# Optimization experiments

Hardware: AMD Instinct MI355X
Metric: run time of the kernel (lower is better)

## Reference

```python
import jax, jax.numpy as jnp
import numpy as np

B, S, I, H = 32, 512, 256, 512  # batch, seq, input, lstm hidden
E = 2 * H                       # embed = hidden*2
NH = 16                         # num heads
HD = E // NH                    # head dim = 64


def setup_inputs() -> dict:
    key = jax.random.key(0)
    ks = jax.random.split(key, 20)
    sI = 1.0 / np.sqrt(I)
    sH = 1.0 / np.sqrt(H)
    sE = 1.0 / np.sqrt(E)
    return {
        "x": jax.random.normal(ks[0], (B, S, I), jnp.float32),
        # LSTM params (PyTorch gate order i,f,g,o); b = b_ih + b_hh folded
        "W_ih_f": jax.random.uniform(ks[1], (4 * H, I), jnp.float32, -sH, sH),
        "W_hh_f": jax.random.uniform(ks[2], (4 * H, H), jnp.float32, -sH, sH),
        "b_f": jax.random.uniform(ks[3], (4 * H,), jnp.float32, -sH, sH),
        "W_ih_b": jax.random.uniform(ks[4], (4 * H, I), jnp.float32, -sH, sH),
        "W_hh_b": jax.random.uniform(ks[5], (4 * H, H), jnp.float32, -sH, sH),
        "b_b": jax.random.uniform(ks[6], (4 * H,), jnp.float32, -sH, sH),
        # attention projections
        "Wq": jax.random.uniform(ks[7], (E, E), jnp.float32, -sE, sE),
        "bq": jax.random.uniform(ks[8], (E,), jnp.float32, -sE, sE),
        "Wk": jax.random.uniform(ks[9], (E, E), jnp.float32, -sE, sE),
        "bk": jax.random.uniform(ks[10], (E,), jnp.float32, -sE, sE),
        "Wv": jax.random.uniform(ks[11], (E, E), jnp.float32, -sE, sE),
        "bv": jax.random.uniform(ks[12], (E,), jnp.float32, -sE, sE),
        "Wo": jax.random.uniform(ks[13], (E, E), jnp.float32, -sE, sE),
        "bo": jax.random.uniform(ks[14], (E,), jnp.float32, -sE, sE),
        # final classifier
        "Wfc": jax.random.uniform(ks[15], (1, E), jnp.float32, -sE, sE),
        "bfc": jax.random.uniform(ks[16], (1,), jnp.float32, -sE, sE),
    }


def _lstm_dir(x, W_ih, W_hh, b, reverse):
    # x: (B,S,I) -> hidden sequence (B,S,H), PyTorch gate order i,f,g,o
    xg = jnp.einsum('bsi,gi->sbg', x, W_ih) + b  # time-major (S,B,4H)
    h0 = jnp.zeros((x.shape[0], W_hh.shape[1]), x.dtype)

    def step(carry, xt):
        h, c = carry
        gates = xt + h @ W_hh.T
        i, f, g, o = jnp.split(gates, 4, axis=-1)
        c = jax.nn.sigmoid(f) * c + jax.nn.sigmoid(i) * jnp.tanh(g)
        h = jax.nn.sigmoid(o) * jnp.tanh(c)
        return (h, c), h

    _, hs = jax.lax.scan(step, (h0, h0), xg, reverse=reverse)
    return jnp.swapaxes(hs, 0, 1)  # (B,S,H)


def reference(x, W_ih_f, W_hh_f, b_f, W_ih_b, W_hh_b, b_b,
              Wq, bq, Wk, bk, Wv, bv, Wo, bo, Wfc, bfc):
    # Bidirectional LSTM
    h_fwd = _lstm_dir(x, W_ih_f, W_hh_f, b_f, reverse=False)
    h_bwd = _lstm_dir(x, W_ih_b, W_hh_b, b_b, reverse=True)
    h = jnp.concatenate([h_fwd, h_bwd], axis=-1)  # (B,S,E)

    # Multi-head attention, replicating the original (label-scrambled) einsums.
    # Q/K/V are reshaped to (N, NH, S, HD) via transpose(1,2) as in torch.
    def proj(W, bias):
        p = h @ W.T + bias                      # (B,S,E)
        return p.reshape(B, S, NH, HD).transpose(0, 2, 1, 3)  # (B,NH,S,HD)

    Q, K, V = proj(Wq, bq), proj(Wk, bk), proj(Wv, bv)
    # torch: einsum('nqhd,nkhd->nhqk', Q, K) with Q,K actually (N,NH,S,HD)
    # => scores shape (B, S, NH, NH), softmax over last (heads) axis
    scores = jnp.einsum('nqhd,nkhd->nhqk', Q, K) / jnp.sqrt(jnp.float32(HD))
    attn = jax.nn.softmax(scores, axis=-1)
    # torch: einsum('nhqk,nkhd->nqhd', attn, V) -> (B, NH, S, HD)
    out = jnp.einsum('nhqk,nkhd->nqhd', attn, V).reshape(B, S, E)
    out = out @ Wo.T + bo                       # (B,S,E)

    # dropout is identity at inference; take last timestep, fc, sigmoid
    last = out[:, -1, :]                        # (B,E)
    return jax.nn.sigmoid(last @ Wfc.T + bfc)   # (B,1)
```

## Files before the change

kernel.cpp:

```cpp
#include <hip/hip_runtime.h>
#include <cstdint>
#include <cstddef>


typedef _Float16 v8h __attribute__((ext_vector_type(8)));
typedef _Float16 v4h __attribute__((ext_vector_type(4)));
typedef float    v4f __attribute__((ext_vector_type(4)));

#define AT_LD(p)     __hip_atomic_load((p), __ATOMIC_RELAXED, __HIP_MEMORY_SCOPE_AGENT)
#define AT_ST(p, v)  __hip_atomic_store((p), (v), __ATOMIC_RELAXED, __HIP_MEMORY_SCOPE_AGENT)

static constexpr size_t OFF_CNT   = 0;
static constexpr size_t OFF_LOGIT = 256;
static constexpr size_t OFF_BEFF  = 512;
static constexpr size_t OFF_WEFF  = 1024;
static constexpr size_t OFF_HF    = 8192;
static constexpr size_t HF_BYTES  = 513ull*32768;
static constexpr size_t OFF_HB    = OFF_HF + HF_BYTES;
static constexpr size_t HB_BYTES  = 17ull*32768;
static constexpr size_t OFF_WHHF  = OFF_HB + HB_BYTES;
static constexpr size_t OFF_WIHF  = OFF_WHHF + 2048ull*512*2;
static constexpr size_t OFF_WHHB  = OFF_WIHF + 2048ull*256*2;
static constexpr size_t OFF_WIHB  = OFF_WHHB + 2048ull*512*2;
static constexpr size_t OFF_WKT   = OFF_WIHB + 2048ull*256*2;
static constexpr size_t OFF_WQT   = OFF_WKT + 1024ull*1024*2;
static constexpr size_t OFF_WV2   = OFF_WQT + 1024ull*64*2;
static constexpr size_t OFF_CV    = OFF_WV2 + 16ull*1024*16*4;

static constexpr int PSTR    = 776;
static constexpr int GSTR    = 68;
static constexpr int LDS_PANEL_B = 16*PSTR*2;
static constexpr int DYN_LDS = LDS_PANEL_B + 64*GSTR*4;

__device__ __forceinline__ bool has_ffff(unsigned long long w) {
    return ((w & 0xFFFFull) == 0xFFFFull) ||
           (((w >> 16) & 0xFFFFull) == 0xFFFFull) ||
           (((w >> 32) & 0xFFFFull) == 0xFFFFull) ||
           ((w >> 48) == 0xFFFFull);
}


__global__ void k_convert(const float* __restrict__ whhf, const float* __restrict__ wihf,
                          const float* __restrict__ whhb, const float* __restrict__ wihb,
                          char* __restrict__ ws)
{
    _Float16* o1 = (_Float16*)(ws + OFF_WHHF);
    _Float16* o2 = (_Float16*)(ws + OFF_WIHF);
    _Float16* o3 = (_Float16*)(ws + OFF_WHHB);
    _Float16* o4 = (_Float16*)(ws + OFF_WIHB);
    const int stride = gridDim.x * blockDim.x;
    for (int i = blockIdx.x*blockDim.x + threadIdx.x; i < 2048*512; i += stride) {
        o1[i] = (_Float16)whhf[i];
        o3[i] = (_Float16)whhb[i];
    }
    for (int i = blockIdx.x*blockDim.x + threadIdx.x; i < 2048*256; i += stride) {
        o2[i] = (_Float16)wihf[i];
        o4[i] = (_Float16)wihb[i];
    }
}

__global__ void k_weff(const float* __restrict__ Wfc, const float* __restrict__ Wo,
                       const float* __restrict__ bo, const float* __restrict__ bfc,
                       char* __restrict__ ws)
{
    float* weff = (float*)(ws + OFF_WEFF);
    float* beff = (float*)(ws + OFF_BEFF);
    const int bid = blockIdx.x;
    const int e2 = (bid & 3)*256 + threadIdx.x;
    const int slab = bid >> 2;
    float a = 0.f;
    for (int e = slab*64; e < slab*64 + 64; ++e)
        a += Wfc[e] * Wo[(size_t)e*1024 + e2];
    atomicAdd(weff + e2, a);
    if ((bid & 3) == 0 && threadIdx.x < 64) {
        const int e = slab*64 + threadIdx.x;
        float b = Wfc[e]*bo[e];
        if (bid == 0 && threadIdx.x == 0) b += bfc[0];
        atomicAdd(beff, b);
    }
}

__global__ void k_wv2(const float* __restrict__ Wv, const float* __restrict__ bv,
                      char* __restrict__ ws)
{
    const float* weff = (const float*)(ws + OFF_WEFF);
    float* wv2 = (float*)(ws + OFF_WV2);
    float* cv  = (float*)(ws + OFF_CV);
    const int bid = blockIdx.x;
    if (bid < 64) {
        const int r = bid >> 2;
        const int e = (bid & 3)*256 + threadIdx.x;
        for (int kh = 0; kh < 16; ++kh) {
            float a = 0.f;
            for (int hd = 0; hd < 64; ++hd)
                a += weff[r*64 + hd] * Wv[((size_t)(kh*64 + hd))*1024 + e];
            wv2[((size_t)r*1024 + e)*16 + kh] = a;
        }
    } else {
        const int r2 = threadIdx.x >> 4, k2 = threadIdx.x & 15;
        float a = 0.f;
        for (int hd = 0; hd < 64; ++hd)
            a += weff[r2*64 + hd] * bv[k2*64 + hd];
        cv[threadIdx.x] = a;
    }
}

__global__ void k_tk(const float* __restrict__ Wk, char* __restrict__ ws)
{
    _Float16* WkT = (_Float16*)(ws + OFF_WKT);
    __shared__ float tile[32][33];
    const int jt = blockIdx.x & 31, et = blockIdx.x >> 5;
    const int tx = threadIdx.x & 31, ty = threadIdx.x >> 5;
    for (int i = 0; i < 4; ++i)
        tile[ty + 8*i][tx] = Wk[((size_t)(jt*32 + ty + 8*i))*1024 + et*32 + tx];
    __syncthreads();
    for (int i = 0; i < 4; ++i)
        WkT[((size_t)(et*32 + ty + 8*i))*1024 + jt*32 + tx] = (_Float16)tile[tx][ty + 8*i];
}

__global__ void k_tq(const float* __restrict__ Wq, char* __restrict__ ws)
{
    _Float16* WqT = (_Float16*)(ws + OFF_WQT);
    const int gid = blockIdx.x*256 + threadIdx.x;
    const int d = gid & 63, e = gid >> 6;
    WqT[e*64 + d] = (_Float16)Wq[((size_t)(960 + d))*1024 + e];
}


__global__ __launch_bounds__(256, 1)
void bilstm_main(const float* __restrict__ xg,
                 const float* __restrict__ b_f, const float* __restrict__ b_b,
                 const float* __restrict__ bq,  const float* __restrict__ bk,
                 char* __restrict__ ws, float* __restrict__ out)
{
    extern __shared__ char smem[];
    _Float16* panel = (_Float16*)smem;
    float* gates = (float*)(smem + LDS_PANEL_B);

    const int tid  = threadIdx.x;
    const int wgid = blockIdx.x;
    const int wave = tid >> 6;
    const int lane = tid & 63;
    const int quad = lane >> 4;
    const int l16  = lane & 15;
    const int grp  = wgid >> 5;
    const int col0 = (wgid & 31) * 16;

    unsigned* cnts  = (unsigned*)(ws + OFF_CNT);
    float*   logits = (float*)(ws + OFF_LOGIT);

    const int ac = tid & 15;
    const int ab = tid >> 4;

    for (int phase = 0; phase < 2; ++phase) {
        const int dir     = phase == 0 ? 1 : 0;
        const int nsteps  = dir ? 16 : 512;
        char* hslab = ws + (dir ? OFF_HB : OFF_HF);
        const _Float16* whh = (const _Float16*)(ws + (dir ? OFF_WHHB : OFF_WHHF));
        const _Float16* wih = (const _Float16*)(ws + (dir ? OFF_WIHB : OFF_WIHF));
        const float* bias = dir ? b_b : b_f;

        v8h bfrag[4][6];
#pragma unroll
        for (int nt = 0; nt < 4; ++nt)
#pragma unroll
            for (int kk = 0; kk < 6; ++kk) {
                const int kb = (wave*6 + kk)*32 + quad*8;
                const int r  = nt*512 + col0 + l16;
                const _Float16* src = (kb < 512) ? (whh + (size_t)r*512 + kb)
                                                 : (wih + (size_t)r*256 + (kb - 512));
                bfrag[nt][kk] = *(const v8h*)src;
            }
        float bia[4];
#pragma unroll
        for (int g = 0; g < 4; ++g) bia[g] = bias[g*512 + col0 + ac];

        float cst = 0.f;

        for (int t = 0; t < nsteps; ++t) {
            const int s = dir ? (511 - t) : t;

            float4 xv[2];
#pragma unroll
            for (int i = 0; i < 2; ++i) {
                const int ch = tid + 256*i;
                const int b = ch >> 6, ic = ch & 63;
                xv[i] = *(const float4*)(xg + ((size_t)(grp*8 + b)*512 + s)*256 + ic*4);
            }

            {
                const int b = tid >> 5, seg = tid & 31;
                const unsigned long long* src = (const unsigned long long*)hslab
                    + (size_t)t*4096 + (size_t)(grp*8 + b)*128 + seg*4;
                unsigned long long w0, w1, w2, w3;
                for (;;) {
                    w0 = AT_LD(src + 0); w1 = AT_LD(src + 1);
                    w2 = AT_LD(src + 2); w3 = AT_LD(src + 3);
                    if (!(has_ffff(w0) || has_ffff(w1) || has_ffff(w2) || has_ffff(w3)))
                        break;
                    __builtin_amdgcn_s_sleep(1);
                }
                unsigned long long* dst = (unsigned long long*)(panel + b*PSTR + seg*16);
                dst[0] = w0; dst[1] = w1; dst[2] = w2; dst[3] = w3;
            }
#pragma unroll
            for (int i = 0; i < 2; ++i) {
                const int ch = tid + 256*i;
                const int b = ch >> 6, ic = ch & 63;
                v4h hx = { (_Float16)xv[i].x, (_Float16)xv[i].y,
                           (_Float16)xv[i].z, (_Float16)xv[i].w };
                *(v4h*)(panel + b*PSTR + 512 + ic*4) = hx;
            }
            __syncthreads();

            v4f acc[4];
#pragma unroll
            for (int nt = 0; nt < 4; ++nt) { v4f z = {0.f,0.f,0.f,0.f}; acc[nt] = z; }
#pragma unroll
            for (int kk = 0; kk < 6; ++kk) {
                const int kb = (wave*6 + kk)*32 + quad*8;
                const v8h a0 = *(const v8h*)(panel + l16*PSTR + kb);
#pragma unroll
                for (int nt = 0; nt < 4; ++nt)
                    acc[nt] = __builtin_amdgcn_mfma_f32_16x16x32_f16(a0, bfrag[nt][kk], acc[nt], 0, 0, 0);
            }
#pragma unroll
            for (int nt = 0; nt < 4; ++nt)
#pragma unroll
                for (int r = 0; r < 4; ++r)
                    gates[(nt*16 + l16)*GSTR + (quad*4 + r)*4 + wave] = acc[nt][r];
            __syncthreads();

            if (tid < 128) {
                float g[4];
#pragma unroll
                for (int gi = 0; gi < 4; ++gi) {
                    const v4f v = *(const v4f*)(gates + (gi*16 + ac)*GSTR + ab*4);
                    g[gi] = v.x + v.y + v.z + v.w + bia[gi];
                }
                const float ig = 1.f/(1.f + __expf(-g[0]));
                const float fg = 1.f/(1.f + __expf(-g[1]));
                const float gg = 1.f - 2.f/(__expf(2.f*g[2]) + 1.f);
                const float og = 1.f/(1.f + __expf(-g[3]));
                cst = fg*cst + ig*gg;
                const float hn = og * (1.f - 2.f/(__expf(2.f*cst) + 1.f));
                const unsigned hb = (unsigned)__builtin_bit_cast(unsigned short, (_Float16)hn);
                const unsigned ot = (unsigned)__shfl_xor((int)hb, 1);
                if ((ac & 1) == 0) {
                    _Float16* hrow = (_Float16*)hslab
                        + ((size_t)(t+1)*32 + (grp*8 + ab))*512 + col0 + ac;
                    AT_ST((unsigned*)hrow, hb | (ot << 16));
                }
            }
        }
    }

    __syncthreads();
    if (tid == 0) {
        __hip_atomic_fetch_add(cnts + 0, 1u, __ATOMIC_RELAXED, __HIP_MEMORY_SCOPE_AGENT);
        while (AT_LD(cnts + 0) < 128u) __builtin_amdgcn_s_sleep(8);
    }
    __syncthreads();

    float*    hv  = (float*)smem;
    _Float16* k16 = (_Float16*)(smem + 16384);
    float*    qb  = (float*)(smem + 24576);
    float*    vzb = (float*)(smem + 25600);
    float*    scb = (float*)(smem + 25856);
    int*      lastf = (int*)(smem + 26112);

    const _Float16* WkT = (const _Float16*)(ws + OFF_WKT);
    const _Float16* WqT = (const _Float16*)(ws + OFF_WQT);
    const float* wv2 = (const float*)(ws + OFF_WV2);
    const float* cv  = (const float*)(ws + OFF_CV);
    const float* beff= (const float*)(ws + OFF_BEFF);

    const int p0 = wgid * 4;
#pragma unroll
    for (int i = 0; i < 4; ++i) {
        const int ch = tid + 256*i;
        const int pp = ch >> 8, q = ch & 255;
        const int p = p0 + pp; const int b = p >> 4; const int r = p & 15;
        unsigned long long w;
        if (q < 128)
            w = AT_LD((const unsigned long long*)(ws + OFF_HF)
                      + ((size_t)(497 + r)*32 + b)*128 + q);
        else
            w = AT_LD((const unsigned long long*)(ws + OFF_HB)
                      + ((size_t)(16 - r)*32 + b)*128 + (q - 128));
        float* dst = hv + pp*1024 + q*4;
#pragma unroll
        for (int j = 0; j < 4; ++j)
            dst[j] = (float)__builtin_bit_cast(_Float16, (unsigned short)((w >> (16*j)) & 0xFFFF));
    }
    __syncthreads();

    float kacc[4][4];
#pragma unroll
    for (int jj = 0; jj < 4; ++jj) {
        const float bkv = bk[jj*256 + tid];
#pragma unroll
        for (int pp = 0; pp < 4; ++pp) kacc[jj][pp] = bkv;
    }
    for (int e = 0; e < 1024; ++e) {
        float hvv[4];
#pragma unroll
        for (int pp = 0; pp < 4; ++pp) hvv[pp] = hv[pp*1024 + e];
#pragma unroll
        for (int jj = 0; jj < 4; ++jj) {
            const float w = (float)WkT[(size_t)e*1024 + jj*256 + tid];
#pragma unroll
            for (int pp = 0; pp < 4; ++pp) kacc[jj][pp] += w * hvv[pp];
        }
    }
#pragma unroll
    for (int jj = 0; jj < 4; ++jj)
#pragma unroll
        for (int pp = 0; pp < 4; ++pp)
            k16[pp*1024 + jj*256 + tid] = (_Float16)kacc[jj][pp];

    {
        const int d = tid & 63, ph = tid >> 6;
        float a0 = bq[960 + d];
        for (int e = 0; e < 1024; ++e)
            a0 += (float)WqT[e*64 + d] * hv[ph*1024 + e];
        qb[ph*64 + d] = a0;
    }
    if (tid < 64) {
        const int pp = tid >> 4, kh = tid & 15;
        const int r = (p0 + pp) & 15;
        float a = cv[r*16 + kh];
        for (int e = 0; e < 1024; ++e)
            a += wv2[((size_t)r*1024 + e)*16 + kh] * hv[pp*1024 + e];
        vzb[pp*16 + kh] = a;
    }
    __syncthreads();
    if (tid < 64) {
        const int pp = tid >> 4, kh = tid & 15;
        float a = 0.f;
#pragma unroll
        for (int d = 0; d < 64; ++d)
            a += qb[pp*64 + d] * (float)k16[pp*1024 + kh*64 + d];
        scb[pp*16 + kh] = a * 0.125f;
    }
    __syncthreads();
    if (tid < 4) {
        const int base = tid*16;
        float m = scb[base];
        for (int kh = 1; kh < 16; ++kh) m = fmaxf(m, scb[base+kh]);
        float sum = 0.f, wz = 0.f;
        for (int kh = 0; kh < 16; ++kh) {
            const float pe = __expf(scb[base+kh] - m);
            sum += pe; wz += pe * vzb[base+kh];
        }
        atomicAdd(&logits[(p0 + tid) >> 4], wz / sum);
    }
    __syncthreads();
    if (tid == 0) {
        const unsigned old = __hip_atomic_fetch_add(cnts + 2, 1u, __ATOMIC_RELAXED, __HIP_MEMORY_SCOPE_AGENT);
        *lastf = (old == 127u) ? 1 : 0;
    }
    __syncthreads();
    if (*lastf) {
        if (tid < 32) {
            const float lg = AT_LD(logits + tid) + beff[0];
            out[tid] = 1.f/(1.f + __expf(-lg));
        }
    }
}


extern "C" void kernel_launch(void* const* d_in, const int* in_sizes, int n_in,
                              void* d_out, int out_size, void* d_ws, size_t ws_size,
                              hipStream_t stream)
{
    (void)in_sizes; (void)n_in; (void)out_size; (void)ws_size;
    const float* x    = (const float*)d_in[0];
    const float* Wihf = (const float*)d_in[1];
    const float* Whhf = (const float*)d_in[2];
    const float* b_f  = (const float*)d_in[3];
    const float* Wihb = (const float*)d_in[4];
    const float* Whhb = (const float*)d_in[5];
    const float* b_b  = (const float*)d_in[6];
    const float* Wq   = (const float*)d_in[7];
    const float* bq   = (const float*)d_in[8];
    const float* Wk   = (const float*)d_in[9];
    const float* bk   = (const float*)d_in[10];
    const float* Wv   = (const float*)d_in[11];
    const float* bv   = (const float*)d_in[12];
    const float* Wo   = (const float*)d_in[13];
    const float* bo   = (const float*)d_in[14];
    const float* Wfc  = (const float*)d_in[15];
    const float* bfc  = (const float*)d_in[16];
    char* ws = (char*)d_ws;
    float* out = (float*)d_out;

    hipMemsetAsync(ws, 0, OFF_HF + 32768, stream);
    hipMemsetAsync(ws + OFF_HF + 32768, 0xFF, 512ull*32768, stream);
    hipMemsetAsync(ws + OFF_HB, 0, 32768, stream);
    hipMemsetAsync(ws + OFF_HB + 32768, 0xFF, 16ull*32768, stream);

    hipLaunchKernelGGL(k_convert, dim3(512), dim3(256), 0, stream, Whhf, Wihf, Whhb, Wihb, ws);
    hipLaunchKernelGGL(k_weff,    dim3(64),  dim3(256), 0, stream, Wfc, Wo, bo, bfc, ws);
    hipLaunchKernelGGL(k_wv2,     dim3(65),  dim3(256), 0, stream, Wv, bv, ws);
    hipLaunchKernelGGL(k_tk,      dim3(1024),dim3(256), 0, stream, Wk, ws);
    hipLaunchKernelGGL(k_tq,      dim3(256), dim3(256), 0, stream, Wq, ws);
    hipLaunchKernelGGL(bilstm_main, dim3(128), dim3(256), DYN_LDS, stream,
                       x, b_f, b_b, bq, bk, ws, out);
}
```

Baseline: 1.853 ms.

## Replace sentinel-polled h slabs with flagged ring buffer and halve workgroups

The recurrent hidden-state exchange no longer uses a full per-timestep slab pre-filled with 0xFFFF sentinels. It now uses a 4-deep ring buffer plus per-step flag words, and each consumer spins on a 64-bit flag pair before reading. The grid drops from 128 to 64 workgroups, each handling 16 batch rows with all 256 threads doing cell updates. The last 16 timesteps are written to a compact history buffer for the attention tail, which removes the large 0xFF memsets. The risks are tighter sync ordering (relying on s_waitcnt plus relaxed atomics), busy-wait loops without sleep, and double the per-workgroup work on the serial critical path.

```diff
diff --git a/kernel.cpp b/kernel.cpp
--- a/kernel.cpp
+++ b/kernel.cpp
@@ -6,6 +6,7 @@
 typedef _Float16 v8h __attribute__((ext_vector_type(8)));
 typedef _Float16 v4h __attribute__((ext_vector_type(4)));
 typedef float    v4f __attribute__((ext_vector_type(4)));
+typedef unsigned long long u64;
 
 #define AT_LD(p)     __hip_atomic_load((p), __ATOMIC_RELAXED, __HIP_MEMORY_SCOPE_AGENT)
 #define AT_ST(p, v)  __hip_atomic_store((p), (v), __ATOMIC_RELAXED, __HIP_MEMORY_SCOPE_AGENT)
@@ -14,11 +15,13 @@
 static constexpr size_t OFF_LOGIT = 256;
 static constexpr size_t OFF_BEFF  = 512;
 static constexpr size_t OFF_WEFF  = 1024;
-static constexpr size_t OFF_HF    = 8192;
-static constexpr size_t HF_BYTES  = 513ull*32768;
-static constexpr size_t OFF_HB    = OFF_HF + HF_BYTES;
-static constexpr size_t HB_BYTES  = 17ull*32768;
-static constexpr size_t OFF_WHHF  = OFF_HB + HB_BYTES;
+static constexpr size_t OFF_FLAGF = 8192;
+static constexpr size_t OFF_FLAGB = OFF_FLAGF + 512ull*64*4;
+static constexpr size_t ZERO_BYTES= OFF_FLAGB + 16ull*64*4;
+static constexpr size_t OFF_RINGF = ZERO_BYTES;
+static constexpr size_t OFF_RINGB = OFF_RINGF + 4ull*2*16*512*2;
+static constexpr size_t OFF_HIST  = OFF_RINGB + 4ull*2*16*512*2;
+static constexpr size_t OFF_WHHF  = OFF_HIST + 32ull*16*1024*4;
 static constexpr size_t OFF_WIHF  = OFF_WHHF + 2048ull*512*2;
 static constexpr size_t OFF_WHHB  = OFF_WIHF + 2048ull*256*2;
 static constexpr size_t OFF_WIHB  = OFF_WHHB + 2048ull*512*2;
@@ -27,17 +30,12 @@
 static constexpr size_t OFF_WV2   = OFF_WQT + 1024ull*64*2;
 static constexpr size_t OFF_CV    = OFF_WV2 + 16ull*1024*16*4;
 
-static constexpr int PSTR    = 776;
-static constexpr int GSTR    = 68;
+static constexpr int PSTR = 776;
+static constexpr int GSTR = 68;
 static constexpr int LDS_PANEL_B = 16*PSTR*2;
-static constexpr int DYN_LDS = LDS_PANEL_B + 64*GSTR*4;
-
-__device__ __forceinline__ bool has_ffff(unsigned long long w) {
-    return ((w & 0xFFFFull) == 0xFFFFull) ||
-           (((w >> 16) & 0xFFFFull) == 0xFFFFull) ||
-           (((w >> 32) & 0xFFFFull) == 0xFFFFull) ||
-           ((w >> 48) == 0xFFFFull);
-}
+static constexpr int LDS_GATES_B = 64*GSTR*4;
+static constexpr int DYN_LDS = 53504;
+static constexpr u64 FLAG_PAIR = 0x0000000100000001ull;
 
 
 __global__ void k_convert(const float* __restrict__ whhf, const float* __restrict__ wihf,
@@ -136,6 +134,7 @@
     extern __shared__ char smem[];
     _Float16* panel = (_Float16*)smem;
     float* gates = (float*)(smem + LDS_PANEL_B);
+    _Float16* hout = (_Float16*)(smem + LDS_PANEL_B + LDS_GATES_B);
 
     const int tid  = threadIdx.x;
     const int wgid = blockIdx.x;
@@ -144,21 +143,25 @@
     const int quad = lane >> 4;
     const int l16  = lane & 15;
     const int grp  = wgid >> 5;
-    const int col0 = (wgid & 31) * 16;
+    const int cg   = wgid & 31;
+    const int col0 = cg * 16;
 
     unsigned* cnts  = (unsigned*)(ws + OFF_CNT);
     float*   logits = (float*)(ws + OFF_LOGIT);
+    float*   hist   = (float*)(ws + OFF_HIST);
 
     const int ac = tid & 15;
     const int ab = tid >> 4;
 
     for (int phase = 0; phase < 2; ++phase) {
-        const int dir     = phase == 0 ? 1 : 0;
-        const int nsteps  = dir ? 16 : 512;
-        char* hslab = ws + (dir ? OFF_HB : OFF_HF);
+        const int dir    = (phase == 0) ? 1 : 0;
+        const int nsteps = dir ? 16 : 512;
+        _Float16* ring = (_Float16*)(ws + (dir ? OFF_RINGB : OFF_RINGF));
+        unsigned* flg  = (unsigned*)(ws + (dir ? OFF_FLAGB : OFF_FLAGF));
         const _Float16* whh = (const _Float16*)(ws + (dir ? OFF_WHHB : OFF_WHHF));
         const _Float16* wih = (const _Float16*)(ws + (dir ? OFF_WIHB : OFF_WIHF));
         const float* bias = dir ? b_b : b_f;
+        const int histoff = dir ? 512 : 0;
 
         v8h bfrag[4][6];
 #pragma unroll
@@ -180,31 +183,32 @@
         for (int t = 0; t < nsteps; ++t) {
             const int s = dir ? (511 - t) : t;
 
-            float4 xv[2];
-#pragma unroll
-            for (int i = 0; i < 2; ++i) {
+            float4 xv[4];
+#pragma unroll
+            for (int i = 0; i < 4; ++i) {
                 const int ch = tid + 256*i;
                 const int b = ch >> 6, ic = ch & 63;
-                xv[i] = *(const float4*)(xg + ((size_t)(grp*8 + b)*512 + s)*256 + ic*4);
-            }
-
-            {
-                const int b = tid >> 5, seg = tid & 31;
-                const unsigned long long* src = (const unsigned long long*)hslab
-                    + (size_t)t*4096 + (size_t)(grp*8 + b)*128 + seg*4;
-                unsigned long long w0, w1, w2, w3;
-                for (;;) {
-                    w0 = AT_LD(src + 0); w1 = AT_LD(src + 1);
-                    w2 = AT_LD(src + 2); w3 = AT_LD(src + 3);
-                    if (!(has_ffff(w0) || has_ffff(w1) || has_ffff(w2) || has_ffff(w3)))
-                        break;
-                    __builtin_amdgcn_s_sleep(1);
-                }
-                unsigned long long* dst = (unsigned long long*)(panel + b*PSTR + seg*16);
-                dst[0] = w0; dst[1] = w1; dst[2] = w2; dst[3] = w3;
-            }
-#pragma unroll
-            for (int i = 0; i < 2; ++i) {
+                xv[i] = *(const float4*)(xg + ((size_t)(grp*16 + b)*512 + s)*256 + ic*4);
+            }
+
+            if (t == 0) {
+                u64* dst = (u64*)(panel + ab*PSTR + ac*32);
+#pragma unroll
+                for (int j = 0; j < 8; ++j) dst[j] = 0ull;
+            } else {
+                const u64* f64 = (const u64*)flg + ((size_t)(t-1)*2 + grp)*16 + ac;
+                while (AT_LD(f64) != FLAG_PAIR) {}
+                const u64* src = (const u64*)ring
+                    + ((((size_t)((t-1) & 3))*2 + grp)*16 + ab)*128 + ac*8;
+                u64 w[8];
+#pragma unroll
+                for (int j = 0; j < 8; ++j) w[j] = AT_LD(src + j);
+                u64* dst = (u64*)(panel + ab*PSTR + ac*32);
+#pragma unroll
+                for (int j = 0; j < 8; ++j) dst[j] = w[j];
+            }
+#pragma unroll
+            for (int i = 0; i < 4; ++i) {
                 const int ch = tid + 256*i;
                 const int b = ch >> 6, ic = ch & 63;
                 v4h hx = { (_Float16)xv[i].x, (_Float16)xv[i].y,
@@ -231,7 +235,7 @@
                     gates[(nt*16 + l16)*GSTR + (quad*4 + r)*4 + wave] = acc[nt][r];
             __syncthreads();
 
-            if (tid < 128) {
+            {
                 float g[4];
 #pragma unroll
                 for (int gi = 0; gi < 4; ++gi) {
@@ -244,13 +248,21 @@
                 const float og = 1.f/(1.f + __expf(-g[3]));
                 cst = fg*cst + ig*gg;
                 const float hn = og * (1.f - 2.f/(__expf(2.f*cst) + 1.f));
-                const unsigned hb = (unsigned)__builtin_bit_cast(unsigned short, (_Float16)hn);
-                const unsigned ot = (unsigned)__shfl_xor((int)hb, 1);
-                if ((ac & 1) == 0) {
-                    _Float16* hrow = (_Float16*)hslab
-                        + ((size_t)(t+1)*32 + (grp*8 + ab))*512 + col0 + ac;
-                    AT_ST((unsigned*)hrow, hb | (ot << 16));
-                }
+                hout[ab*16 + ac] = (_Float16)hn;
+                if (s >= 496)
+                    AT_ST(hist + ((size_t)(grp*16 + ab)*16 + (s - 496))*1024
+                               + histoff + col0 + ac, hn);
+            }
+            __syncthreads();
+
+            if (wave == 0) {
+                const int b = lane >> 2, seg = lane & 3;
+                const u64 v = *(const u64*)(hout + b*16 + seg*4);
+                AT_ST((u64*)(ring + ((((size_t)(t & 3))*2 + grp)*16 + b)*512
+                             + col0 + seg*4), v);
+                asm volatile("s_waitcnt vmcnt(0)" ::: "memory");
+                if (lane == 0)
+                    AT_ST(flg + ((size_t)t*2 + grp)*32 + cg, 1u);
             }
         }
     }
@@ -258,16 +270,16 @@
     __syncthreads();
     if (tid == 0) {
         __hip_atomic_fetch_add(cnts + 0, 1u, __ATOMIC_RELAXED, __HIP_MEMORY_SCOPE_AGENT);
-        while (AT_LD(cnts + 0) < 128u) __builtin_amdgcn_s_sleep(8);
+        while (AT_LD(cnts + 0) < 64u) {}
     }
     __syncthreads();
 
     float*    hv  = (float*)smem;
-    _Float16* k16 = (_Float16*)(smem + 16384);
-    float*    qb  = (float*)(smem + 24576);
-    float*    vzb = (float*)(smem + 25600);
-    float*    scb = (float*)(smem + 25856);
-    int*      lastf = (int*)(smem + 26112);
+    _Float16* k16 = (_Float16*)(smem + 32768);
+    float*    qb  = (float*)(smem + 49152);
+    float*    vzb = (float*)(smem + 51200);
+    float*    scb = (float*)(smem + 51712);
+    int*      lastf = (int*)(smem + 53248);
 
     const _Float16* WkT = (const _Float16*)(ws + OFF_WKT);
     const _Float16* WqT = (const _Float16*)(ws + OFF_WQT);
@@ -275,58 +287,56 @@
     const float* cv  = (const float*)(ws + OFF_CV);
     const float* beff= (const float*)(ws + OFF_BEFF);
 
-    const int p0 = wgid * 4;
-#pragma unroll
-    for (int i = 0; i < 4; ++i) {
-        const int ch = tid + 256*i;
-        const int pp = ch >> 8, q = ch & 255;
-        const int p = p0 + pp; const int b = p >> 4; const int r = p & 15;
-        unsigned long long w;
-        if (q < 128)
-            w = AT_LD((const unsigned long long*)(ws + OFF_HF)
-                      + ((size_t)(497 + r)*32 + b)*128 + q);
-        else
-            w = AT_LD((const unsigned long long*)(ws + OFF_HB)
-                      + ((size_t)(16 - r)*32 + b)*128 + (q - 128));
-        float* dst = hv + pp*1024 + q*4;
-#pragma unroll
-        for (int j = 0; j < 4; ++j)
-            dst[j] = (float)__builtin_bit_cast(_Float16, (unsigned short)((w >> (16*j)) & 0xFFFF));
-    }
-    __syncthreads();
-
-    float kacc[4][4];
+    const int p0 = wgid * 8;
+    {
+        const u64* hist64 = (const u64*)hist;
+#pragma unroll
+        for (int i = 0; i < 16; ++i) {
+            const int ch = tid + 256*i;
+            const int pp = ch >> 9, e2 = ch & 511;
+            const int p = p0 + pp; const int b = p >> 4, r = p & 15;
+            const u64 w = AT_LD(hist64 + ((size_t)b*16 + r)*512 + e2);
+            *(u64*)(hv + pp*1024 + e2*2) = w;
+        }
+    }
+    __syncthreads();
+
+    float kacc[4][8];
 #pragma unroll
     for (int jj = 0; jj < 4; ++jj) {
         const float bkv = bk[jj*256 + tid];
 #pragma unroll
-        for (int pp = 0; pp < 4; ++pp) kacc[jj][pp] = bkv;
+        for (int pp = 0; pp < 8; ++pp) kacc[jj][pp] = bkv;
     }
     for (int e = 0; e < 1024; ++e) {
-        float hvv[4];
-#pragma unroll
-        for (int pp = 0; pp < 4; ++pp) hvv[pp] = hv[pp*1024 + e];
+        float hvv[8];
+#pragma unroll
+        for (int pp = 0; pp < 8; ++pp) hvv[pp] = hv[pp*1024 + e];
 #pragma unroll
         for (int jj = 0; jj < 4; ++jj) {
             const float w = (float)WkT[(size_t)e*1024 + jj*256 + tid];
 #pragma unroll
-            for (int pp = 0; pp < 4; ++pp) kacc[jj][pp] += w * hvv[pp];
+            for (int pp = 0; pp < 8; ++pp) kacc[jj][pp] += w * hvv[pp];
         }
     }
 #pragma unroll
     for (int jj = 0; jj < 4; ++jj)
 #pragma unroll
-        for (int pp = 0; pp < 4; ++pp)
+        for (int pp = 0; pp < 8; ++pp)
             k16[pp*1024 + jj*256 + tid] = (_Float16)kacc[jj][pp];
 
     {
         const int d = tid & 63, ph = tid >> 6;
-        float a0 = bq[960 + d];
-        for (int e = 0; e < 1024; ++e)
-            a0 += (float)WqT[e*64 + d] * hv[ph*1024 + e];
+        float a0 = bq[960 + d], a1 = a0;
+        for (int e = 0; e < 1024; ++e) {
+            const float w = (float)WqT[e*64 + d];
+            a0 += w * hv[ph*1024 + e];
+            a1 += w * hv[(ph+4)*1024 + e];
+        }
         qb[ph*64 + d] = a0;
-    }
-    if (tid < 64) {
+        qb[(ph+4)*64 + d] = a1;
+    }
+    if (tid < 128) {
         const int pp = tid >> 4, kh = tid & 15;
         const int r = (p0 + pp) & 15;
         float a = cv[r*16 + kh];
@@ -335,7 +345,7 @@
         vzb[pp*16 + kh] = a;
     }
     __syncthreads();
-    if (tid < 64) {
+    if (tid < 128) {
         const int pp = tid >> 4, kh = tid & 15;
         float a = 0.f;
 #pragma unroll
@@ -344,7 +354,7 @@
         scb[pp*16 + kh] = a * 0.125f;
     }
     __syncthreads();
-    if (tid < 4) {
+    if (tid < 8) {
         const int base = tid*16;
         float m = scb[base];
         for (int kh = 1; kh < 16; ++kh) m = fmaxf(m, scb[base+kh]);
@@ -357,8 +367,8 @@
     }
     __syncthreads();
     if (tid == 0) {
-        const unsigned old = __hip_atomic_fetch_add(cnts + 2, 1u, __ATOMIC_RELAXED, __HIP_MEMORY_SCOPE_AGENT);
-        *lastf = (old == 127u) ? 1 : 0;
+        const unsigned old = __hip_atomic_fetch_add(cnts + 1, 1u, __ATOMIC_RELAXED, __HIP_MEMORY_SCOPE_AGENT);
+        *lastf = (old == 63u) ? 1 : 0;
     }
     __syncthreads();
     if (*lastf) {
@@ -395,16 +405,12 @@
     char* ws = (char*)d_ws;
     float* out = (float*)d_out;
 
-    hipMemsetAsync(ws, 0, OFF_HF + 32768, stream);
-    hipMemsetAsync(ws + OFF_HF + 32768, 0xFF, 512ull*32768, stream);
-    hipMemsetAsync(ws + OFF_HB, 0, 32768, stream);
-    hipMemsetAsync(ws + OFF_HB + 32768, 0xFF, 16ull*32768, stream);
-
+    hipMemsetAsync(ws, 0, ZERO_BYTES, stream);
     hipLaunchKernelGGL(k_convert, dim3(512), dim3(256), 0, stream, Whhf, Wihf, Whhb, Wihb, ws);
     hipLaunchKernelGGL(k_weff,    dim3(64),  dim3(256), 0, stream, Wfc, Wo, bo, bfc, ws);
     hipLaunchKernelGGL(k_wv2,     dim3(65),  dim3(256), 0, stream, Wv, bv, ws);
     hipLaunchKernelGGL(k_tk,      dim3(1024),dim3(256), 0, stream, Wk, ws);
     hipLaunchKernelGGL(k_tq,      dim3(256), dim3(256), 0, stream, Wq, ws);
-    hipLaunchKernelGGL(bilstm_main, dim3(128), dim3(256), DYN_LDS, stream,
+    hipLaunchKernelGGL(bilstm_main, dim3(64), dim3(256), DYN_LDS, stream,
                        x, b_f, b_b, bq, bk, ws, out);
 }
```

Result: slower. 2.156 ms (+16.3%).
